# Kernel tuning notes

Hardware: AMD Instinct MI355X
Metric: run time of the kernel (lower is better)

Reference implementation:

```python
import jax, jax.numpy as jnp
import numpy as np

B = 8
A = 180      # num_angles
D = 512      # det_count
IMG = 512    # img_size


def _forward(x):
    # --- Ram-Lak filter in frequency domain ---
    freq = jnp.abs(jnp.fft.rfftfreq(D)).astype(jnp.float32)            # [D//2+1]
    filtered = jnp.fft.irfft(jnp.fft.rfft(x, axis=-1) * freq, n=D, axis=-1)  # [B,A,D]

    # --- precompute per-angle detector coordinates for every pixel ---
    lin = jnp.linspace(-1.0, 1.0, IMG, dtype=jnp.float32)
    yy, xx = jnp.meshgrid(lin, lin, indexing='ij')
    xxf = xx.reshape(-1)                                               # [HW]
    yyf = yy.reshape(-1)
    angles = jnp.linspace(0.0, np.pi - np.pi / A, A, dtype=jnp.float32)
    t = (xxf[None, :] * jnp.cos(angles)[:, None]
         + yyf[None, :] * jnp.sin(angles)[:, None]) / np.sqrt(2.0)     # [A,HW]
    u = jnp.clip((t + 1.0) * 0.5 * (D - 1.0), 0.0, D - 1.0)
    idx0 = jnp.floor(u).astype(jnp.int32)
    idx1 = jnp.minimum(idx0 + 1, D - 1)
    w = u - idx0.astype(jnp.float32)

    # --- backprojection sweep: scan over angles, accumulate in-register ---
    proj = jnp.transpose(filtered, (1, 0, 2))                          # [A,B,D]

    def step(acc, inputs):
        p, i0, i1, wa = inputs                                         # p:[B,D], i*/wa:[HW]
        s = jnp.take(p, i0, axis=1) * (1.0 - wa) + jnp.take(p, i1, axis=1) * wa
        return acc + s, None

    bn = x.shape[0]
    acc0 = jnp.zeros((bn, IMG * IMG), dtype=jnp.float32)
    acc, _ = jax.lax.scan(step, acc0, (proj, idx0, idx1, w))

    det_pixel_size = 2.0 / float(D)
    fbp = acc.reshape(bn, 1, IMG, IMG) * (det_pixel_size * np.pi / float(A))

    # --- 3x3 gaussian blur (sigma=0.5), depthwise on single channel ---
    coords = jnp.arange(-1, 2, dtype=jnp.float32)
    k1 = jnp.exp(-0.5 * (coords / 0.5) ** 2)
    k1 = k1 / k1.sum()
    k2 = jnp.outer(k1, k1)[None, None]                                 # [1,1,3,3] OIHW
    fbp = jax.lax.conv_general_dilated(fbp, k2, (1, 1), 'SAME')
    return jnp.clip(fbp, -1.0, 1.0)


def setup_inputs() -> dict:
    key = jax.random.key(0)
    x = jax.random.normal(key, (B, A, D), dtype=jnp.float32)
    return {"x": x, "input_is_sinogram": 1}


def reference(x, input_is_sinogram):
    # input_is_sinogram is a constant flag (True path): x is the sinogram [B,A,D].
    return _forward(x)
```

## Files before the change

kernel.cpp:

```cpp
#include <hip/hip_runtime.h>
#include <hip/hip_fp16.h>
#include <math.h>

#define NDET 512
#define NANG 180
#define NB   8
#define NIMG 512

#define WS_CASA 0
#define WS_CBT  360
#define WS_FGA  46440
#define WS_FGB  (46440 + 368640)

typedef _Float16 h2_t __attribute__((ext_vector_type(2)));

__device__ __forceinline__ void gld_lds16(const void* g, void* l) {
    __builtin_amdgcn_global_load_lds((__attribute__((address_space(1))) void*)g,
                                     (__attribute__((address_space(3))) void*)l,
                                     16, 0, 0);
}

__device__ __forceinline__ int hswz(int s) {
    return (s & 0x78) | ((s ^ (s >> 3)) & 7);
}

__global__ __launch_bounds__(512) void k_filter(const float* __restrict__ x, float* ws) {
    __shared__ float xs[8 * 516];
    __shared__ float hrs[512];
    __shared__ float fsm[512 * 8];
    const int a    = blockIdx.x;
    const int tid  = threadIdx.x;
    const int lane = tid & 63;
    const int wv   = tid >> 6;

    {
        const float* xr = x + (wv * NANG + a) * NDET;
        gld_lds16(xr + lane * 4,       xs + wv * 516 + lane * 4);
        gld_lds16(xr + 256 + lane * 4, xs + wv * 516 + 256 + lane * 4);
    }
    {
        int n = tid;
        float h;
        if (n == 0) h = 0.25f;
        else if ((n & 1) == 0) h = 0.0f;
        else {
            int m = min(n, 512 - n);
            float s = __sinf((float)m * (float)(M_PI / 512.0));
            h = -1.0f / (262144.0f * s * s);
        }
        hrs[hswz(n >> 2) * 4 + (n & 3)] = h;
    }
    if (tid == 0) {
        double th = (double)a * (M_PI / 180.0);
        double sc = 255.5 / sqrt(2.0);
        ws[WS_CASA + 2 * a]     = (float)(cos(th) * sc);
        ws[WS_CASA + 2 * a + 1] = (float)(sin(th) * sc);
    }
    if (tid < 256) {
        double th = (double)a * (M_PI / 180.0);
        double sc = 255.5 / sqrt(2.0);
        const float cad = (float)(cos(th) * sc), sad = (float)(sin(th) * sc);
        const int bx = tid & 15, by = tid >> 4;
        const float x0 = -1.f + (float)(bx * 32 - 1)  * (2.f / 511.f);
        const float x1 = -1.f + (float)(bx * 32 + 32) * (2.f / 511.f);
        const float y0 = -1.f + (float)(by * 32 - 1)  * (2.f / 511.f);
        const float y1 = -1.f + (float)(by * 32 + 32) * (2.f / 511.f);
        float u00 = fmaf(x0, cad, fmaf(y0, sad, 255.5f));
        float u01 = fmaf(x1, cad, fmaf(y0, sad, 255.5f));
        float u10 = fmaf(x0, cad, fmaf(y1, sad, 255.5f));
        float u11 = fmaf(x1, cad, fmaf(y1, sad, 255.5f));
        float umin = fminf(fminf(u00, u01), fminf(u10, u11));
        int d0 = (int)floorf(umin);
        d0 = max(0, min(NDET - 35, d0));
        ws[WS_CBT + tid * 180 + a] = 255.5f - (float)d0;
    }
    __syncthreads();

    {
        const int b  = lane & 7;
        const int t  = lane >> 3;
        const int n0 = wv * 64 + t * 8;
        const int q  = n0 >> 2;
        const float* xrow = xs + b * 516;

        float acc[8] = {0, 0, 0, 0, 0, 0, 0, 0};
        float win[12];
        {
            int s2 = (-q - 2) & 127;
            int s1 = (-q - 1) & 127;
            float4 h2 = *(const float4*)(hrs + hswz(s2) * 4);
            float4 h1 = *(const float4*)(hrs + hswz(s1) * 4);
            win[0] = h2.x; win[1] = h2.y; win[2]  = h2.z; win[3]  = h2.w;
            win[4] = h1.x; win[5] = h1.y; win[6]  = h1.z; win[7]  = h1.w;
        }
        #pragma unroll 4
        for (int c = 0; c < 128; ++c) {
            int s = (c - q) & 127;
            float4 hc = *(const float4*)(hrs + hswz(s) * 4);
            win[8] = hc.x; win[9] = hc.y; win[10] = hc.z; win[11] = hc.w;
            float4 xv = *(const float4*)(xrow + c * 4);
            float xa[4] = {xv.x, xv.y, xv.z, xv.w};
            #pragma unroll
            for (int k = 0; k < 8; ++k)
                #pragma unroll
                for (int j = 0; j < 4; ++j)
                    acc[k] = fmaf(xa[j], win[8 + j - k], acc[k]);
            #pragma unroll
            for (int i2 = 0; i2 < 8; ++i2) win[i2] = win[i2 + 4];
        }
        #pragma unroll
        for (int k = 0; k < 8; ++k)
            fsm[(n0 + k) * 8 + b] = acc[k];
    }
    __syncthreads();
    {
        const int d  = tid;
        const int d1 = min(d + 1, NDET - 1);
        const float* A  = fsm + d * 8;
        const float* Bv = fsm + d1 * 8;
        uint4 eA, eB;
        unsigned wds[8];
        #pragma unroll
        for (int b = 0; b < 8; ++b) {
            __half2 h;
            h.x = __float2half(A[b]);
            h.y = __float2half(Bv[b]);
            wds[b] = __builtin_bit_cast(unsigned, h);
        }
        eA.x = wds[0]; eA.y = wds[1]; eA.z = wds[2]; eA.w = wds[3];
        eB.x = wds[4]; eB.y = wds[5]; eB.z = wds[6]; eB.w = wds[7];
        *(uint4*)((char*)(ws + WS_FGA) + (a * NDET + d) * 16) = eA;
        *(uint4*)((char*)(ws + WS_FGB) + (a * NDET + d) * 16) = eB;
    }
}

#define WWE  34
#define CHA  60
#define ECH  (CHA * WWE)

__global__ __launch_bounds__(1024, 4) void k_bp(float* ws, float* __restrict__ out) {
    __shared__ uint4 win4[2][2 * ECH];
    __shared__ float casal[2 * NANG];
    __shared__ float cbl[NANG];
    const int tid  = threadIdx.x;
    const int wv   = tid >> 6, lane = tid & 63;
    const int tile = blockIdx.x;
    const int bx   = tile & 15, by = tile >> 4;

    const int iy1 = (wv >> 2) * 8 + (lane >> 3);
    const int ix1 = (wv & 3) * 8 + (lane & 7);
    const int lx1 = ix1 + 1, ly1 = iy1 + 1;
    const float xf1 = -1.0f + (float)(bx * 32 + ix1) * (2.0f / 511.0f);
    const float yf1 = -1.0f + (float)(by * 32 + iy1) * (2.0f / 511.0f);

    const bool has2 = (tid < 132);
    int lx2, ly2;
    {
        const int i = tid;
        if (i < 34)       { lx2 = i;        ly2 = 0;       }
        else if (i < 68)  { lx2 = i - 34;   ly2 = 33;      }
        else if (i < 100) { lx2 = 0;        ly2 = i - 67;  }
        else              { lx2 = 33;       ly2 = i - 99;  }
    }
    const int gx2 = bx * 32 - 1 + lx2, gy2 = by * 32 - 1 + ly2;
    const bool in2 = has2 && (gx2 >= 0) && (gx2 < NIMG) && (gy2 >= 0) && (gy2 < NIMG);
    const float xf2 = -1.0f + (float)gx2 * (2.0f / 511.0f);
    const float yf2 = -1.0f + (float)gy2 * (2.0f / 511.0f);

    const char* __restrict__ fga = (const char*)(ws + WS_FGA);
    const char* __restrict__ fgb = (const char*)(ws + WS_FGB);

    if (tid < NANG) {
        cbl[tid] = ws[WS_CBT + tile * 180 + tid];
        casal[2 * tid]     = ws[WS_CASA + 2 * tid];
        casal[2 * tid + 1] = ws[WS_CASA + 2 * tid + 1];
    }
    __syncthreads();

    auto stageq = [&](int buf, int ch) {
        #pragma unroll
        for (int r = 0; r < 4; ++r) {
            int c = r * 1024 + tid;
            if (c < 2 * ECH) {
                int reg = c / ECH;
                int e   = c - reg * ECH;
                int a   = e / WWE;
                int o   = e - a * WWE;
                int ag  = ch * CHA + a;
                int d0  = (int)(255.5f - cbl[ag]);
                const char* g = (reg ? fgb : fga) + (ag * NDET + d0 + o) * 16;
                gld_lds16(g, (char*)(&win4[buf][0]) + c * 16);
            }
        }
    };

    float acc1[8] = {0, 0, 0, 0, 0, 0, 0, 0};
    float acc2[8] = {0, 0, 0, 0, 0, 0, 0, 0};
    auto comp = [&](int buf, int ch, float xf, float yf, float* acc) {
        #pragma unroll 4
        for (int al = 0; al < CHA; ++al) {
            const int ag = ch * CHA + al;
            const float ca = casal[2 * ag], sa = casal[2 * ag + 1];
            const float cb = cbl[ag];
            float v = fmaf(xf, ca, fmaf(yf, sa, cb));
            v = __builtin_amdgcn_fmed3f(v, 0.0f, 33.99996948f);
            float fj = floorf(v);
            float w  = v - fj;
            int  j0  = (int)fj;
            uint4 dA = win4[buf][al * WWE + j0];
            uint4 dB = win4[buf][ECH + al * WWE + j0];
            h2_t wp = __builtin_bit_cast(h2_t, __builtin_amdgcn_cvt_pkrtz(1.0f - w, w));
            acc[0] = __builtin_amdgcn_fdot2(__builtin_bit_cast(h2_t, dA.x), wp, acc[0], false);
            acc[1] = __builtin_amdgcn_fdot2(__builtin_bit_cast(h2_t, dA.y), wp, acc[1], false);
            acc[2] = __builtin_amdgcn_fdot2(__builtin_bit_cast(h2_t, dA.z), wp, acc[2], false);
            acc[3] = __builtin_amdgcn_fdot2(__builtin_bit_cast(h2_t, dA.w), wp, acc[3], false);
            acc[4] = __builtin_amdgcn_fdot2(__builtin_bit_cast(h2_t, dB.x), wp, acc[4], false);
            acc[5] = __builtin_amdgcn_fdot2(__builtin_bit_cast(h2_t, dB.y), wp, acc[5], false);
            acc[6] = __builtin_amdgcn_fdot2(__builtin_bit_cast(h2_t, dB.z), wp, acc[6], false);
            acc[7] = __builtin_amdgcn_fdot2(__builtin_bit_cast(h2_t, dB.w), wp, acc[7], false);
        }
    };

    stageq(0, 0); __syncthreads();
    stageq(1, 1);
    comp(0, 0, xf1, yf1, acc1);
    if (has2) comp(0, 0, xf2, yf2, acc2);
    __syncthreads();
    stageq(0, 2);
    comp(1, 1, xf1, yf1, acc1);
    if (has2) comp(1, 1, xf2, yf2, acc2);
    __syncthreads();
    comp(0, 2, xf1, yf1, acc1);
    if (has2) comp(0, 2, xf2, yf2, acc2);

    const float scale = (float)((2.0 / 512.0) * M_PI / 180.0);
    const float KA = 0.10650697891920077f;
    const float KB = 0.78698604216159850f;
    float* grid = (float*)&win4[0][0];
    const int ixl = (tid & 31) + 1, iyl = (tid >> 5) + 1;
    const int ogx = bx * 32 + (tid & 31), ogy = by * 32 + (tid >> 5);

    #pragma unroll
    for (int b = 0; b < 8; ++b) {
        __syncthreads();
        grid[ly1 * 35 + lx1] = acc1[b] * scale;
        if (has2) grid[ly2 * 35 + lx2] = in2 ? acc2[b] * scale : 0.0f;
        __syncthreads();
        const float* g0 = grid + (iyl - 1) * 35 + ixl;
        const float* g1 = grid + iyl * 35 + ixl;
        const float* g2 = grid + (iyl + 1) * 35 + ixl;
        float rowm = KA * (g0[-1] + g0[1]) + KB * g0[0];
        float row0 = KA * (g1[-1] + g1[1]) + KB * g1[0];
        float rowp = KA * (g2[-1] + g2[1]) + KB * g2[0];
        float v = KA * (rowm + rowp) + KB * row0;
        v = fminf(fmaxf(v, -1.0f), 1.0f);
        out[b * (NIMG * NIMG) + ogy * NIMG + ogx] = v;
    }
}

extern "C" void kernel_launch(void* const* d_in, const int* in_sizes, int n_in,
                              void* d_out, int out_size, void* d_ws, size_t ws_size,
                              hipStream_t stream) {
    const float* x = (const float*)d_in[0];
    float* out = (float*)d_out;
    float* ws  = (float*)d_ws;

    k_filter<<<NANG, 512, 0, stream>>>(x, ws);
    k_bp<<<256, 1024, 0, stream>>>(ws, out);
}
```

Measured before the change: 62.98 us.

## Stage only half of projection windows in LDS, read other half from global

Replaces the double-buffered, chunked LDS staging of both fp16 projection halves with a single upfront load of all angles' A-half window into LDS. The B half (batches 4-7) is now gathered directly from global memory inside the per-angle loop. This removes the intermediate barriers and staging pipeline, but it adds per-pixel, per-angle 16-byte global gathers that depend on cache hits and have higher latency.

After: 71.61 us. +13.7%, slower.

```diff
diff --git a/kernel.cpp b/kernel.cpp
--- a/kernel.cpp
+++ b/kernel.cpp
@@ -135,11 +135,9 @@
 }
 
 #define WWE  34
-#define CHA  60
-#define ECH  (CHA * WWE)
 
 __global__ __launch_bounds__(1024, 4) void k_bp(float* ws, float* __restrict__ out) {
-    __shared__ uint4 win4[2][2 * ECH];
+    __shared__ uint4 winA[NANG * WWE];
     __shared__ float casal[2 * NANG];
     __shared__ float cbl[NANG];
     const int tid  = threadIdx.x;
@@ -167,48 +165,42 @@
     const float xf2 = -1.0f + (float)gx2 * (2.0f / 511.0f);
     const float yf2 = -1.0f + (float)gy2 * (2.0f / 511.0f);
 
-    const char* __restrict__ fga = (const char*)(ws + WS_FGA);
-    const char* __restrict__ fgb = (const char*)(ws + WS_FGB);
-
+    const char*  __restrict__ fga  = (const char*)(ws + WS_FGA);
+    const char*  __restrict__ fgb  = (const char*)(ws + WS_FGB);
+    const float* __restrict__ cbtg = ws + WS_CBT + tile * 180;
+
+    #pragma unroll
+    for (int r = 0; r < 6; ++r) {
+        int c = r * 1024 + tid;
+        if (c < NANG * WWE) {
+            int a = c / WWE;
+            int o = c - a * WWE;
+            int d0 = (int)(255.5f - cbtg[a]);
+            gld_lds16(fga + (a * NDET + d0 + o) * 16, winA + c);
+        }
+    }
     if (tid < NANG) {
-        cbl[tid] = ws[WS_CBT + tile * 180 + tid];
+        cbl[tid] = cbtg[tid];
         casal[2 * tid]     = ws[WS_CASA + 2 * tid];
         casal[2 * tid + 1] = ws[WS_CASA + 2 * tid + 1];
     }
     __syncthreads();
 
-    auto stageq = [&](int buf, int ch) {
-        #pragma unroll
-        for (int r = 0; r < 4; ++r) {
-            int c = r * 1024 + tid;
-            if (c < 2 * ECH) {
-                int reg = c / ECH;
-                int e   = c - reg * ECH;
-                int a   = e / WWE;
-                int o   = e - a * WWE;
-                int ag  = ch * CHA + a;
-                int d0  = (int)(255.5f - cbl[ag]);
-                const char* g = (reg ? fgb : fga) + (ag * NDET + d0 + o) * 16;
-                gld_lds16(g, (char*)(&win4[buf][0]) + c * 16);
-            }
-        }
-    };
-
     float acc1[8] = {0, 0, 0, 0, 0, 0, 0, 0};
     float acc2[8] = {0, 0, 0, 0, 0, 0, 0, 0};
-    auto comp = [&](int buf, int ch, float xf, float yf, float* acc) {
+    auto comp = [&](float xf, float yf, float* acc) {
         #pragma unroll 4
-        for (int al = 0; al < CHA; ++al) {
-            const int ag = ch * CHA + al;
-            const float ca = casal[2 * ag], sa = casal[2 * ag + 1];
-            const float cb = cbl[ag];
+        for (int al = 0; al < NANG; ++al) {
+            const float ca = casal[2 * al], sa = casal[2 * al + 1];
+            const float cb = cbl[al];
             float v = fmaf(xf, ca, fmaf(yf, sa, cb));
             v = __builtin_amdgcn_fmed3f(v, 0.0f, 33.99996948f);
             float fj = floorf(v);
             float w  = v - fj;
             int  j0  = (int)fj;
-            uint4 dA = win4[buf][al * WWE + j0];
-            uint4 dB = win4[buf][ECH + al * WWE + j0];
+            const int d0 = (int)(255.5f - cb);
+            uint4 dA = winA[al * WWE + j0];
+            uint4 dB = *(const uint4*)(fgb + (al * NDET + d0 + j0) * 16);
             h2_t wp = __builtin_bit_cast(h2_t, __builtin_amdgcn_cvt_pkrtz(1.0f - w, w));
             acc[0] = __builtin_amdgcn_fdot2(__builtin_bit_cast(h2_t, dA.x), wp, acc[0], false);
             acc[1] = __builtin_amdgcn_fdot2(__builtin_bit_cast(h2_t, dA.y), wp, acc[1], false);
@@ -221,22 +213,13 @@
         }
     };
 
-    stageq(0, 0); __syncthreads();
-    stageq(1, 1);
-    comp(0, 0, xf1, yf1, acc1);
-    if (has2) comp(0, 0, xf2, yf2, acc2);
-    __syncthreads();
-    stageq(0, 2);
-    comp(1, 1, xf1, yf1, acc1);
-    if (has2) comp(1, 1, xf2, yf2, acc2);
-    __syncthreads();
-    comp(0, 2, xf1, yf1, acc1);
-    if (has2) comp(0, 2, xf2, yf2, acc2);
+    comp(xf1, yf1, acc1);
+    if (has2) comp(xf2, yf2, acc2);
 
     const float scale = (float)((2.0 / 512.0) * M_PI / 180.0);
     const float KA = 0.10650697891920077f;
     const float KB = 0.78698604216159850f;
-    float* grid = (float*)&win4[0][0];
+    float* grid = (float*)&winA[0];
     const int ixl = (tid & 31) + 1, iyl = (tid >> 5) + 1;
     const int ogx = bx * 32 + (tid & 31), ogy = by * 32 + (tid >> 5);
 
```
